# Optimization experiments

Hardware: AMD Instinct MI355X
Metric: run time of the kernel (lower is better)

## Reference

```python
import jax, jax.numpy as jnp
import numpy as np


def setup_inputs() -> dict:
    key = jax.random.key(0)
    k1, k2 = jax.random.split(key)
    B, H, W, D, K = 32, 64, 64, 64, 512
    inputs = jax.random.normal(k1, (B, H, W, D), dtype=jnp.float32)
    # codebook: (D, K) as in the keras layer (embedding_dim x num_embeddings)
    embeddings = jax.random.uniform(k2, (D, K), dtype=jnp.float32,
                                    minval=-1.0, maxval=1.0) * (3.0 / D) ** 0.5
    return {"inputs": inputs, "embeddings": embeddings}


def reference(inputs, embeddings):
    # inputs: [B, H, W, D]; embeddings: [D, K]
    D = inputs.shape[-1]
    flat = inputs.reshape(-1, D)                                   # [N, D]
    distances = (jnp.sum(flat * flat, axis=1, keepdims=True)
                 - 2.0 * (flat @ embeddings)
                 + jnp.sum(embeddings * embeddings, axis=0, keepdims=True))
    encoding_indices = jnp.argmin(distances, axis=1)               # [N]
    encoding_indices = encoding_indices.reshape(inputs.shape[:-1])  # [B, H, W]
    quantized = jnp.take(embeddings.T, encoding_indices, axis=0)   # [B, H, W, D]
    # straight-through estimator
    return inputs + jax.lax.stop_gradient(quantized - inputs)
```

## Files before the change

### kernel.cpp

```cpp
#include <hip/hip_runtime.h>


#define KC 512
#define DD 64
#define TAU 5e-4f
#define HTAU (0.5f * TAU)

typedef __attribute__((ext_vector_type(8))) short short8;
typedef __attribute__((ext_vector_type(4))) float float4v;

__device__ inline unsigned short f2bf(float f) {
    unsigned u = __float_as_uint(f);
    return (unsigned short)((u + 0x7FFF + ((u >> 16) & 1)) >> 16);
}
__device__ inline float bf2f(unsigned short b) {
    return __uint_as_float((unsigned)b << 16);
}

__global__ __launch_bounds__(256) void vq_prep(const float* __restrict__ emb,
                                               float* __restrict__ et,
                                               float* __restrict__ bias,
                                               short* __restrict__ Bh,
                                               short* __restrict__ Bl) {
    __shared__ float tile[DD][17];
    const int ct = blockIdx.x;
    const int t  = threadIdx.x;

    {
        const int d = t >> 2, c0 = (t & 3) * 4;
        float4 v = *(const float4*)(emb + (size_t)d * KC + ct * 16 + c0);
        tile[d][c0 + 0] = v.x; tile[d][c0 + 1] = v.y;
        tile[d][c0 + 2] = v.z; tile[d][c0 + 3] = v.w;
    }
    __syncthreads();

    if (t < 16) {
        float s = 0.f;
        #pragma unroll
        for (int d = 0; d < DD; ++d) { float v = tile[d][t]; s += v * v; }
        bias[ct * 16 + t] = s;
    }

    {
        const int c = t >> 4, d0 = (t & 15) * 4;
        float4 v;
        v.x = tile[d0 + 0][c]; v.y = tile[d0 + 1][c];
        v.z = tile[d0 + 2][c]; v.w = tile[d0 + 3][c];
        *(float4*)(et + (size_t)(ct * 16 + c) * DD + d0) = v;
    }

    {
        const int term = t >> 7;
        const int kc   = (t >> 6) & 1;
        const int l    = t & 63;
        const int c    = l & 15, dq = l >> 4;
        short v8[8];
        #pragma unroll
        for (int j = 0; j < 8; ++j) {
            float f = tile[kc * 32 + dq * 8 + j][c];
            unsigned short h = f2bf(f);
            v8[j] = (short)(term == 0 ? h : f2bf(f - bf2f(h)));
        }
        short* dst = (term == 0 ? Bh : Bl) + ((size_t)(ct * 2 + kc) * 64 + l) * 8;
        *(short8*)dst = *(short8*)v8;
    }
}

__global__ __launch_bounds__(1024, 4) void vq_main(const float* __restrict__ x_in,
                                                   const short* __restrict__ Bh,
                                                   const short* __restrict__ Bl,
                                                   const float* __restrict__ bias,
                                                   const float* __restrict__ et,
                                                   float* __restrict__ out) {
    __shared__ __align__(16) short Bh_lds[32 * 2 * 64 * 8];
    __shared__ __align__(16) short Bl_lds[32 * 2 * 64 * 8];
    __shared__ float bias_s[KC];
    __shared__ int   k1s[16][32];
    __shared__ float gaps[16][32];

    const int t = threadIdx.x, w = t >> 6, l = t & 63;
    const int col = l & 15, quad = l >> 4;
    const int R0 = blockIdx.x * 512;
    const int wrow0 = w * 32;

    {
        const float4* srcH = (const float4*)Bh;
        const float4* srcL = (const float4*)Bl;
        float4* dstH = (float4*)Bh_lds;
        float4* dstL = (float4*)Bl_lds;
        #pragma unroll
        for (int j = 0; j < 4; ++j) {
            const int idx = t + j * 1024;
            dstH[idx] = srcH[idx];
            dstL[idx] = srcL[idx];
        }
        if (t < KC) bias_s[t] = bias[t];
    }

    short8 AH[2][2], AL[2][2];
    #pragma unroll
    for (int rt = 0; rt < 2; ++rt)
        #pragma unroll
        for (int kc = 0; kc < 2; ++kc) {
            const float* p = x_in + (size_t)(R0 + wrow0 + rt * 16 + col) * DD
                           + kc * 32 + quad * 8;
            float4 xa = *(const float4*)p;
            float4 xb = *(const float4*)(p + 4);
            float f[8] = {xa.x, xa.y, xa.z, xa.w, xb.x, xb.y, xb.z, xb.w};
            short8 hi8, lo8;
            #pragma unroll
            for (int j = 0; j < 8; ++j) {
                unsigned short h = f2bf(f[j]);
                hi8[j] = (short)h;
                lo8[j] = (short)f2bf(f[j] - bf2f(h));
            }
            AH[rt][kc] = hi8;
            AL[rt][kc] = lo8;
        }
    __syncthreads();

    float m1[2][4], m2[2][4];
    int   kb[2][4];
    #pragma unroll
    for (int rt = 0; rt < 2; ++rt)
        #pragma unroll
        for (int r = 0; r < 4; ++r) {
            m1[rt][r] = -3.4e38f; m2[rt][r] = -3.4e38f; kb[rt][r] = 0;
        }

    const int ct0 = 2 * w;
    #pragma unroll 2
    for (int i = 0; i < 32; ++i) {
        const int ct = (i + ct0) & 31;
        short8 bh0 = *(const short8*)&Bh_lds[((ct * 2 + 0) * 64 + l) * 8];
        short8 bh1 = *(const short8*)&Bh_lds[((ct * 2 + 1) * 64 + l) * 8];
        short8 bl0 = *(const short8*)&Bl_lds[((ct * 2 + 0) * 64 + l) * 8];
        short8 bl1 = *(const short8*)&Bl_lds[((ct * 2 + 1) * 64 + l) * 8];
        const float ci = -0.5f * bias_s[ct * 16 + col];
        const int kk = ct * 16 + col;
        #pragma unroll
        for (int rt = 0; rt < 2; ++rt) {
            float4v c = {ci, ci, ci, ci};
            c = __builtin_amdgcn_mfma_f32_16x16x32_bf16(AH[rt][0], bh0, c, 0, 0, 0);
            c = __builtin_amdgcn_mfma_f32_16x16x32_bf16(AH[rt][1], bh1, c, 0, 0, 0);
            c = __builtin_amdgcn_mfma_f32_16x16x32_bf16(AL[rt][0], bh0, c, 0, 0, 0);
            c = __builtin_amdgcn_mfma_f32_16x16x32_bf16(AL[rt][1], bh1, c, 0, 0, 0);
            c = __builtin_amdgcn_mfma_f32_16x16x32_bf16(AH[rt][0], bl0, c, 0, 0, 0);
            c = __builtin_amdgcn_mfma_f32_16x16x32_bf16(AH[rt][1], bl1, c, 0, 0, 0);
            #pragma unroll
            for (int r = 0; r < 4; ++r) {
                float cr = c[r];
                bool gt = cr > m1[rt][r];
                m2[rt][r] = fmaxf(fminf(cr, m1[rt][r]), m2[rt][r]);
                kb[rt][r] = gt ? kk : kb[rt][r];
                m1[rt][r] = fmaxf(m1[rt][r], cr);
            }
        }
    }

    #pragma unroll
    for (int rt = 0; rt < 2; ++rt)
        #pragma unroll
        for (int r = 0; r < 4; ++r) {
            float b1 = m1[rt][r], b2 = m2[rt][r];
            int   bk = kb[rt][r];
            #pragma unroll
            for (int m = 1; m <= 8; m <<= 1) {
                float o1 = __shfl_xor(b1, m, 64);
                float o2 = __shfl_xor(b2, m, 64);
                int   ok = __shfl_xor(bk, m, 64);
                float n2 = fmaxf(fmaxf(b2, o2), fminf(b1, o1));
                bool take = (o1 > b1) || (o1 == b1 && ok < bk);
                b1 = take ? o1 : b1;
                bk = take ? ok : bk;
                b2 = n2;
            }
            if (col == 0) {
                const int rowl = rt * 16 + quad * 4 + r;
                k1s[w][rowl]  = bk;
                gaps[w][rowl] = b1 - b2;
            }
        }
    __syncthreads();

    {
        unsigned long long mask = __ballot((l < 32) && (gaps[w][l & 31] <= HTAU));
        mask &= 0xFFFFFFFFull;
        while (mask) {
            const int rr = __builtin_ctzll(mask);
            mask &= mask - 1;
            const size_t grow = (size_t)(R0 + wrow0 + rr) * DD;
            const int kbase = l * 8;
            float acc[8];
            #pragma unroll
            for (int j = 0; j < 8; ++j) acc[j] = 0.f;
            for (int d0 = 0; d0 < DD; d0 += 4) {
                float4 xv = *(const float4*)(x_in + grow + d0);
                #pragma unroll
                for (int j = 0; j < 8; ++j) {
                    float4 ev = *(const float4*)(et + (size_t)(kbase + j) * DD + d0);
                    acc[j] += xv.x * ev.x;
                    acc[j] += xv.y * ev.y;
                    acc[j] += xv.z * ev.z;
                    acc[j] += xv.w * ev.w;
                }
            }
            float4 b0 = *(const float4*)(bias + kbase);
            float4 b1v = *(const float4*)(bias + kbase + 4);
            float bb[8] = {b0.x, b0.y, b0.z, b0.w, b1v.x, b1v.y, b1v.z, b1v.w};
            float bv = 3.4e38f; int bk = 0;
            #pragma unroll
            for (int j = 0; j < 8; ++j) {
                float s = bb[j] - 2.f * acc[j];
                if (s < bv) { bv = s; bk = kbase + j; }
            }
            #pragma unroll
            for (int m = 1; m <= 32; m <<= 1) {
                float ov = __shfl_xor(bv, m, 64);
                int   ok = __shfl_xor(bk, m, 64);
                if (ov < bv || (ov == bv && ok < bk)) { bv = ov; bk = ok; }
            }
            if (l == 0) k1s[w][rr] = bk;
        }
    }

    {
        const int c4 = col * 4;
        #pragma unroll
        for (int i = 0; i < 8; ++i) {
            const int rowl = i * 4 + quad;
            const int bk = k1s[w][rowl];
            float4 v = *(const float4*)(et + (size_t)bk * DD + c4);
            *(float4*)(out + (size_t)(R0 + wrow0 + rowl) * DD + c4) = v;
        }
    }
}

extern "C" void kernel_launch(void* const* d_in, const int* in_sizes, int n_in,
                              void* d_out, int out_size, void* d_ws, size_t ws_size,
                              hipStream_t stream) {
    const float* x_in = (const float*)d_in[0];
    const float* emb  = (const float*)d_in[1];
    float* out = (float*)d_out;

    float* et   = (float*)d_ws;
    float* bias = et + KC * DD;
    short* Bh   = (short*)(bias + KC);
    short* Bl   = Bh + 32 * 2 * 64 * 8;

    const int N = out_size / DD;

    vq_prep<<<32, 256, 0, stream>>>(emb, et, bias, Bh, Bl);
    vq_main<<<N / 512, 1024, 0, stream>>>(x_in, Bh, Bl, bias, et, out);
}
```

Measured before the change: 125.4 us.

## Halve block size and stream codebook into LDS in two halves

Blocks shrink from 1024 to 512 threads and each covers 256 rows. The codebook fragments now load into LDS in two 256-entry halves, with a barrier-guarded reload between them, so LDS per block is halved and more blocks can be resident per CU. The per-wave rotated column start is dropped, and the barrier after writing per-wave argmin results is removed because each wave only reads its own rows. The cost is an extra mid-loop reload and synchronisation, plus the codebook being loaded into LDS by twice as many blocks.

```diff
diff --git a/kernel.cpp b/kernel.cpp
--- a/kernel.cpp
+++ b/kernel.cpp
@@ -66,21 +66,21 @@
     }
 }
 
-__global__ __launch_bounds__(1024, 4) void vq_main(const float* __restrict__ x_in,
-                                                   const short* __restrict__ Bh,
-                                                   const short* __restrict__ Bl,
-                                                   const float* __restrict__ bias,
-                                                   const float* __restrict__ et,
-                                                   float* __restrict__ out) {
-    __shared__ __align__(16) short Bh_lds[32 * 2 * 64 * 8];
-    __shared__ __align__(16) short Bl_lds[32 * 2 * 64 * 8];
+__global__ __launch_bounds__(512, 4) void vq_main(const float* __restrict__ x_in,
+                                                  const short* __restrict__ Bh,
+                                                  const short* __restrict__ Bl,
+                                                  const float* __restrict__ bias,
+                                                  const float* __restrict__ et,
+                                                  float* __restrict__ out) {
+    __shared__ __align__(16) short Bh_lds[16 * 2 * 64 * 8];
+    __shared__ __align__(16) short Bl_lds[16 * 2 * 64 * 8];
     __shared__ float bias_s[KC];
-    __shared__ int   k1s[16][32];
-    __shared__ float gaps[16][32];
+    __shared__ int   k1s[8][32];
+    __shared__ float gaps[8][32];
 
     const int t = threadIdx.x, w = t >> 6, l = t & 63;
     const int col = l & 15, quad = l >> 4;
-    const int R0 = blockIdx.x * 512;
+    const int R0 = blockIdx.x * 256;
     const int wrow0 = w * 32;
 
     {
@@ -90,11 +90,11 @@
         float4* dstL = (float4*)Bl_lds;
         #pragma unroll
         for (int j = 0; j < 4; ++j) {
-            const int idx = t + j * 1024;
+            const int idx = t + j * 512;
             dstH[idx] = srcH[idx];
             dstL[idx] = srcL[idx];
         }
-        if (t < KC) bias_s[t] = bias[t];
+        bias_s[t] = bias[t];
     }
 
     short8 AH[2][2], AL[2][2];
@@ -128,32 +128,48 @@
             m1[rt][r] = -3.4e38f; m2[rt][r] = -3.4e38f; kb[rt][r] = 0;
         }
 
-    const int ct0 = 2 * w;
-    #pragma unroll 2
-    for (int i = 0; i < 32; ++i) {
-        const int ct = (i + ct0) & 31;
-        short8 bh0 = *(const short8*)&Bh_lds[((ct * 2 + 0) * 64 + l) * 8];
-        short8 bh1 = *(const short8*)&Bh_lds[((ct * 2 + 1) * 64 + l) * 8];
-        short8 bl0 = *(const short8*)&Bl_lds[((ct * 2 + 0) * 64 + l) * 8];
-        short8 bl1 = *(const short8*)&Bl_lds[((ct * 2 + 1) * 64 + l) * 8];
-        const float ci = -0.5f * bias_s[ct * 16 + col];
-        const int kk = ct * 16 + col;
-        #pragma unroll
-        for (int rt = 0; rt < 2; ++rt) {
-            float4v c = {ci, ci, ci, ci};
-            c = __builtin_amdgcn_mfma_f32_16x16x32_bf16(AH[rt][0], bh0, c, 0, 0, 0);
-            c = __builtin_amdgcn_mfma_f32_16x16x32_bf16(AH[rt][1], bh1, c, 0, 0, 0);
-            c = __builtin_amdgcn_mfma_f32_16x16x32_bf16(AL[rt][0], bh0, c, 0, 0, 0);
-            c = __builtin_amdgcn_mfma_f32_16x16x32_bf16(AL[rt][1], bh1, c, 0, 0, 0);
-            c = __builtin_amdgcn_mfma_f32_16x16x32_bf16(AH[rt][0], bl0, c, 0, 0, 0);
-            c = __builtin_amdgcn_mfma_f32_16x16x32_bf16(AH[rt][1], bl1, c, 0, 0, 0);
-            #pragma unroll
-            for (int r = 0; r < 4; ++r) {
-                float cr = c[r];
-                bool gt = cr > m1[rt][r];
-                m2[rt][r] = fmaxf(fminf(cr, m1[rt][r]), m2[rt][r]);
-                kb[rt][r] = gt ? kk : kb[rt][r];
-                m1[rt][r] = fmaxf(m1[rt][r], cr);
+    #pragma unroll 1
+    for (int h = 0; h < 2; ++h) {
+        if (h == 1) {
+            __syncthreads();
+            const float4* srcH = (const float4*)Bh + 2048;
+            const float4* srcL = (const float4*)Bl + 2048;
+            float4* dstH = (float4*)Bh_lds;
+            float4* dstL = (float4*)Bl_lds;
+            #pragma unroll
+            for (int j = 0; j < 4; ++j) {
+                const int idx = t + j * 512;
+                dstH[idx] = srcH[idx];
+                dstL[idx] = srcL[idx];
+            }
+            __syncthreads();
+        }
+
+        #pragma unroll 2
+        for (int ctl = 0; ctl < 16; ++ctl) {
+            short8 bh0 = *(const short8*)&Bh_lds[((ctl * 2 + 0) * 64 + l) * 8];
+            short8 bh1 = *(const short8*)&Bh_lds[((ctl * 2 + 1) * 64 + l) * 8];
+            short8 bl0 = *(const short8*)&Bl_lds[((ctl * 2 + 0) * 64 + l) * 8];
+            short8 bl1 = *(const short8*)&Bl_lds[((ctl * 2 + 1) * 64 + l) * 8];
+            const int kk = h * 256 + ctl * 16 + col;
+            const float ci = -0.5f * bias_s[kk];
+            #pragma unroll
+            for (int rt = 0; rt < 2; ++rt) {
+                float4v c = {ci, ci, ci, ci};
+                c = __builtin_amdgcn_mfma_f32_16x16x32_bf16(AH[rt][0], bh0, c, 0, 0, 0);
+                c = __builtin_amdgcn_mfma_f32_16x16x32_bf16(AH[rt][1], bh1, c, 0, 0, 0);
+                c = __builtin_amdgcn_mfma_f32_16x16x32_bf16(AL[rt][0], bh0, c, 0, 0, 0);
+                c = __builtin_amdgcn_mfma_f32_16x16x32_bf16(AL[rt][1], bh1, c, 0, 0, 0);
+                c = __builtin_amdgcn_mfma_f32_16x16x32_bf16(AH[rt][0], bl0, c, 0, 0, 0);
+                c = __builtin_amdgcn_mfma_f32_16x16x32_bf16(AH[rt][1], bl1, c, 0, 0, 0);
+                #pragma unroll
+                for (int r = 0; r < 4; ++r) {
+                    float cr = c[r];
+                    bool gt = cr > m1[rt][r];
+                    m2[rt][r] = fmaxf(fminf(cr, m1[rt][r]), m2[rt][r]);
+                    kb[rt][r] = gt ? kk : kb[rt][r];
+                    m1[rt][r] = fmaxf(m1[rt][r], cr);
+                }
             }
         }
     }
@@ -181,7 +197,6 @@
                 gaps[w][rowl] = b1 - b2;
             }
         }
-    __syncthreads();
 
     {
         unsigned long long mask = __ballot((l < 32) && (gaps[w][l & 31] <= HTAU));
@@ -251,5 +266,5 @@
     const int N = out_size / DD;
 
     vq_prep<<<32, 256, 0, stream>>>(emb, et, bias, Bh, Bl);
-    vq_main<<<N / 512, 1024, 0, stream>>>(x_in, Bh, Bl, bias, et, out);
-}
+    vq_main<<<N / 256, 512, 0, stream>>>(x_in, Bh, Bl, bias, et, out);
+}
```

New measurement: 119.9 us. 4.4% less time.
